# Kernel optimization log

Measured on AMD Instinct MI355X. Metric: run time of the kernel, lower is better.

The kernel has to match this reference:

```python
import jax, jax.numpy as jnp
import numpy as np

C, H, W = 16, 128, 128   # in_features, dim0, dim1
FD, OUT, POOL = 3, 64, 2  # filter_dim, out_features, pooling
B = 32


def setup_inputs() -> dict:
    key = jax.random.key(0)
    k1, k2, k3 = jax.random.split(key, 3)
    x = jax.random.normal(k1, (B, C, H, W), dtype=jnp.float32)
    # linear_layer: weight (in*fd^2, out) scaled by 1/sqrt(in*fd^2), bias (out,)
    weight = jax.random.normal(k2, (C * FD * FD, OUT), dtype=jnp.float32) / jnp.sqrt(
        jnp.float32(C * FD * FD))
    bias = jax.random.normal(k3, (OUT,), dtype=jnp.float32)
    return {"x": x, "weight": weight, "bias": bias}


def reference(x, weight, bias):
    # The one-hot isometry tensordot + reshape is exactly im2col with patch
    # vector ordering c*FD^2 + n*FD + m, so the whole convolution() equals a
    # VALID conv with kernel[o, c, n, m] = weight[c*FD^2 + n*FD + m, o].
    kernel = weight.reshape(C, FD, FD, OUT).transpose(3, 0, 1, 2)  # OIHW
    y = jax.lax.conv_general_dilated(
        x, kernel, window_strides=(1, 1), padding='VALID',
        dimension_numbers=('NCHW', 'OIHW', 'NCHW'))  # (B, OUT, n_conv, m_conv)
    y = jax.nn.relu(y + bias[None, :, None, None])
    b, o, hc, wc = y.shape  # hc = H-FD+1 = 126
    # block max-pool POOLxPOOL (crop to multiple of POOL, as in the original)
    hp, wp = hc // POOL, wc // POOL
    y = y[:, :, :hp * POOL, :wp * POOL].reshape(b, o, hp, POOL, wp, POOL)
    y = jnp.max(y, axis=(3, 5))  # (B, OUT, hp, wp)
    return y.reshape(b, o, -1)  # (B, OUT, hp*wp)
```

## Files before the change

kernel.cpp:

```cpp
#include <hip/hip_runtime.h>


typedef _Float16 f16x8 __attribute__((ext_vector_type(8)));
typedef float f32x16 __attribute__((ext_vector_type(16)));

#define MFMA16(A, B, C) __builtin_amdgcn_mfma_f32_32x32x16_f16(A, B, C, 0, 0, 0)
#define XH_BYTES 16777216

#define GLOAD_LDS16(g, l)                                                    \
  __builtin_amdgcn_global_load_lds(                                          \
      (const __attribute__((address_space(1))) void*)(g),                    \
      (__attribute__((address_space(3))) void*)(l), 16, 0, 0)

__global__ void convert_xw(const float* __restrict__ x,
                           const float* __restrict__ weight,
                           char* __restrict__ ws) {
  const int n = blockIdx.x;
  if (n < 4096) {
    const int g = n * 256 + threadIdx.x;
    const int hf = g & 1, col = (g >> 1) & 127, row = (g >> 8) & 127, b = g >> 15;
    _Float16 h[8];
#pragma unroll
    for (int j = 0; j < 8; ++j)
      h[j] = (_Float16)x[((b * 16 + hf * 8 + j) * 128 + row) * 128 + col];
    *(f16x8*)(ws + g * 16) = *(f16x8*)h;
  } else {
    const int tau = (n - 4096) * 256 + threadIdx.x;
    if (tau >= 1152) return;
    const int t = tau >> 7, r = tau & 127, o = r >> 1, hf = r & 1;
    _Float16 h[8];
#pragma unroll
    for (int j = 0; j < 8; ++j)
      h[j] = (_Float16)weight[((hf * 8 + j) * 9 + t) * 64 + o];
    const int off = (t * 2 + (o >> 5)) * 1024 + (hf * 32 + (o & 31)) * 16;
    *(f16x8*)(ws + XH_BYTES + off) = *(f16x8*)h;
  }
}

__global__ __launch_bounds__(256, 3)
void convpool_main(const char* __restrict__ ws, const float* __restrict__ bias,
                   float* __restrict__ out) {
  __shared__ __align__(16) char lds[41024];
  const int tid = threadIdx.x;
  const int s = blockIdx.x;
  const int b = blockIdx.y;
  const int nsteps = (s < 15) ? 4 : 3;
  const int rb = 8 * s;
  const int lane = tid & 63;
  const int ph = tid >> 6;
  const int half = lane >> 5;
  const int c31 = lane & 31;

  const char* xrow = ws + (size_t)(b * 128 + rb) * 4096 + tid * 16;
#pragma unroll
  for (int r = 0; r < 10; ++r)
    if (rb + r < 128)
      GLOAD_LDS16(xrow + r * 4096, lds + r * 4096 + tid * 16);

  const char* wsW = ws + XH_BYTES;
  f16x8 W[9][2];
#pragma unroll
  for (int t = 0; t < 9; ++t)
#pragma unroll
    for (int ot = 0; ot < 2; ++ot)
      W[t][ot] = *(const f16x8*)(wsW + (t * 2 + ot) * 1024 + lane * 16);

  __syncthreads();

  const int xoff = (ph * 32 + c31) * 32 + half * 16;
  const int pw = ph * 16 + (c31 >> 1);
  const bool doit = ((c31 & 1) == 0) && (pw < 63);

  for (int i = 0; i < nsteps; ++i) {
    f32x16 acc[2][2];
#pragma unroll
    for (int q = 0; q < 16; ++q) {
      acc[0][0][q] = 0.f; acc[0][1][q] = 0.f;
      acc[1][0][q] = 0.f; acc[1][1][q] = 0.f;
    }
    __builtin_amdgcn_s_setprio(1);
#pragma unroll
    for (int t = 0; t < 9; ++t) {
      const int n = t / 3, m = t - 3 * n;
      const int a0 = (2 * i + n) * 4096 + xoff + m * 32;
      f16x8 X0 = *(const f16x8*)(lds + a0);
      f16x8 X1 = *(const f16x8*)(lds + a0 + 4096);
      acc[0][0] = MFMA16(W[t][0], X0, acc[0][0]);
      acc[1][0] = MFMA16(W[t][1], X0, acc[1][0]);
      acc[0][1] = MFMA16(W[t][0], X1, acc[0][1]);
      acc[1][1] = MFMA16(W[t][1], X1, acc[1][1]);
    }
    __builtin_amdgcn_s_setprio(0);

    const int p = 4 * s + i;
    const int obase = ((b * 64) * 63 + p) * 63 + pw;
#pragma unroll
    for (int ot = 0; ot < 2; ++ot)
#pragma unroll
      for (int q = 0; q < 16; ++q) {
        const int o0 = ot * 32 + (q & 3) + 8 * (q >> 2);
        float v = fmaxf(acc[ot][0][q], acc[ot][1][q]);
        v = fmaxf(v, __shfl_xor(v, 1, 64));
        const float bv = half ? bias[o0 + 4] : bias[o0];
        v = fmaxf(v + bv, 0.0f);
        if (doit) out[obase + (o0 + 4 * half) * 3969] = v;
      }
  }
}

extern "C" void kernel_launch(void* const* d_in, const int* in_sizes, int n_in,
                              void* d_out, int out_size, void* d_ws, size_t ws_size,
                              hipStream_t stream) {
  const float* x = (const float*)d_in[0];
  const float* wgt = (const float*)d_in[1];
  const float* bias = (const float*)d_in[2];
  float* out = (float*)d_out;
  char* ws = (char*)d_ws;
  convert_xw<<<dim3(4101), 256, 0, stream>>>(x, wgt, ws);
  convpool_main<<<dim3(16, 32), 256, 0, stream>>>(ws, bias, out);
}
```

Baseline: 44.07 us.

## Split conv-pool blocks across output-channel halves and smaller row strips

Restructures the work split of the main conv-pool kernel. Each block now handles one half of the output channels and a 4-row input strip (2 pooled rows) instead of all 64 channels over 8 rows, which quadruples the grid to 64x32 blocks. LDS per block shrinks and the launch-bounds occupancy hint rises from 3 to 4, aiming for more waves per CU and better latency hiding. In exchange, input rows are loaded redundantly by the two channel-half blocks and by overlapping strips, adding more global/LDS traffic per unit of output.

```diff
diff --git a/kernel.cpp b/kernel.cpp
--- a/kernel.cpp
+++ b/kernel.cpp
@@ -37,15 +37,17 @@
   }
 }
 
-__global__ __launch_bounds__(256, 3)
+__global__ __launch_bounds__(256, 4)
 void convpool_main(const char* __restrict__ ws, const float* __restrict__ bias,
                    float* __restrict__ out) {
-  __shared__ __align__(16) char lds[41024];
+  __shared__ __align__(16) char lds[24640];
   const int tid = threadIdx.x;
-  const int s = blockIdx.x;
+  const int bx = blockIdx.x;
+  const int oh = bx >> 5;
+  const int s = bx & 31;
   const int b = blockIdx.y;
-  const int nsteps = (s < 15) ? 4 : 3;
-  const int rb = 8 * s;
+  const int nsteps = (s < 31) ? 2 : 1;
+  const int rb = 4 * s;
   const int lane = tid & 63;
   const int ph = tid >> 6;
   const int half = lane >> 5;
@@ -53,17 +55,15 @@
 
   const char* xrow = ws + (size_t)(b * 128 + rb) * 4096 + tid * 16;
 #pragma unroll
-  for (int r = 0; r < 10; ++r)
+  for (int r = 0; r < 6; ++r)
     if (rb + r < 128)
       GLOAD_LDS16(xrow + r * 4096, lds + r * 4096 + tid * 16);
 
   const char* wsW = ws + XH_BYTES;
-  f16x8 W[9][2];
+  f16x8 W[9];
 #pragma unroll
   for (int t = 0; t < 9; ++t)
-#pragma unroll
-    for (int ot = 0; ot < 2; ++ot)
-      W[t][ot] = *(const f16x8*)(wsW + (t * 2 + ot) * 1024 + lane * 16);
+    W[t] = *(const f16x8*)(wsW + (t * 2 + oh) * 1024 + lane * 16);
 
   __syncthreads();
 
@@ -72,39 +72,32 @@
   const bool doit = ((c31 & 1) == 0) && (pw < 63);
 
   for (int i = 0; i < nsteps; ++i) {
-    f32x16 acc[2][2];
+    f32x16 a0, a1;
 #pragma unroll
-    for (int q = 0; q < 16; ++q) {
-      acc[0][0][q] = 0.f; acc[0][1][q] = 0.f;
-      acc[1][0][q] = 0.f; acc[1][1][q] = 0.f;
-    }
+    for (int q = 0; q < 16; ++q) { a0[q] = 0.f; a1[q] = 0.f; }
     __builtin_amdgcn_s_setprio(1);
 #pragma unroll
     for (int t = 0; t < 9; ++t) {
       const int n = t / 3, m = t - 3 * n;
-      const int a0 = (2 * i + n) * 4096 + xoff + m * 32;
-      f16x8 X0 = *(const f16x8*)(lds + a0);
-      f16x8 X1 = *(const f16x8*)(lds + a0 + 4096);
-      acc[0][0] = MFMA16(W[t][0], X0, acc[0][0]);
-      acc[1][0] = MFMA16(W[t][1], X0, acc[1][0]);
-      acc[0][1] = MFMA16(W[t][0], X1, acc[0][1]);
-      acc[1][1] = MFMA16(W[t][1], X1, acc[1][1]);
+      const int ad = (2 * i + n) * 4096 + xoff + m * 32;
+      f16x8 X0 = *(const f16x8*)(lds + ad);
+      f16x8 X1 = *(const f16x8*)(lds + ad + 4096);
+      a0 = MFMA16(W[t], X0, a0);
+      a1 = MFMA16(W[t], X1, a1);
     }
     __builtin_amdgcn_s_setprio(0);
 
-    const int p = 4 * s + i;
+    const int p = 2 * s + i;
     const int obase = ((b * 64) * 63 + p) * 63 + pw;
 #pragma unroll
-    for (int ot = 0; ot < 2; ++ot)
-#pragma unroll
-      for (int q = 0; q < 16; ++q) {
-        const int o0 = ot * 32 + (q & 3) + 8 * (q >> 2);
-        float v = fmaxf(acc[ot][0][q], acc[ot][1][q]);
-        v = fmaxf(v, __shfl_xor(v, 1, 64));
-        const float bv = half ? bias[o0 + 4] : bias[o0];
-        v = fmaxf(v + bv, 0.0f);
-        if (doit) out[obase + (o0 + 4 * half) * 3969] = v;
-      }
+    for (int q = 0; q < 16; ++q) {
+      const int o0 = oh * 32 + (q & 3) + 8 * (q >> 2);
+      float v = fmaxf(a0[q], a1[q]);
+      v = fmaxf(v, __shfl_xor(v, 1, 64));
+      const float bv = half ? bias[o0 + 4] : bias[o0];
+      v = fmaxf(v + bv, 0.0f);
+      if (doit) out[obase + (o0 + 4 * half) * 3969] = v;
+    }
   }
 }
 
@@ -117,5 +110,5 @@
   float* out = (float*)d_out;
   char* ws = (char*)d_ws;
   convert_xw<<<dim3(4101), 256, 0, stream>>>(x, wgt, ws);
-  convpool_main<<<dim3(16, 32), 256, 0, stream>>>(ws, bias, out);
+  convpool_main<<<dim3(64, 32), 256, 0, stream>>>(ws, bias, out);
 }
```

Result: faster. 39.02 us (-11.4%).
